# Kernel tuning notes

Measured on AMD Instinct MI355X. Metric: run time of the kernel, lower is better.

Reference implementation:

```python
import jax, jax.numpy as jnp
import numpy as np


def _ste_binarize(w):
    # tanh + (binary - tanh).detach()  ->  forward: (tanh(w) > 0) == (w > 0) as 0/1 float
    t = jnp.tanh(w)
    b = (t > 0).astype(w.dtype)
    return t + jax.lax.stop_gradient(b - t)


def setup_inputs() -> dict:
    key = jax.random.key(0)
    k1, k2, k3 = jax.random.split(key, 3)
    B, S, D_IN, D_OUT = 8, 2048, 4096, 4096
    x = jax.random.normal(k1, (B, S, D_IN), dtype=jnp.float32)
    # nn.Linear default init: U(-1/sqrt(in), 1/sqrt(in))
    bound = 1.0 / np.sqrt(D_IN)
    w_pos = jax.random.uniform(k2, (D_OUT, D_IN), minval=-bound, maxval=bound, dtype=jnp.float32)
    w_neg = jax.random.uniform(k3, (D_OUT, D_IN), minval=-bound, maxval=bound, dtype=jnp.float32)
    return {"x": x, "w_pos": w_pos, "w_neg": w_neg}


def reference(x, w_pos, w_neg):
    wp = _ste_binarize(w_pos)  # [O, I] 0/1 values
    wn = _ste_binarize(w_neg)
    # y = x @ wp.T - x @ wn.T ; fuse the subtract into one GEMM-equivalent expr
    y_pos = jnp.einsum('bsi,oi->bso', x, wp)
    y_neg = jnp.einsum('bsi,oi->bso', x, wn)
    return y_pos - y_neg
```

## Files before the change

kernel.cpp:

```cpp
#include <hip/hip_runtime.h>
#include <stdint.h>


#define M_DIM 16384
#define N_DIM 4096
#define K_DIM 4096

#define BM 256
#define BN 256
#define BK 32
#define NT (K_DIM / BK)
#define SLOT_U16 16384
#define LDS_BYTES 131072

typedef unsigned short u16;
typedef __attribute__((ext_vector_type(8))) __bf16 bf16x8;
typedef __attribute__((ext_vector_type(4))) float f32x4;

__device__ __forceinline__ u16 f2bf(float f) {
    unsigned u = __float_as_uint(f);
    u += 0x7FFFu + ((u >> 16) & 1u);
    return (u16)(u >> 16);
}

__global__ void cvt_x_kernel(const float4* __restrict__ x, uint2* __restrict__ xb, int n4) {
    int i = blockIdx.x * 256 + threadIdx.x;
    if (i >= n4) return;
    float4 v = x[i];
    uint2 r;
    r.x = (unsigned)f2bf(v.x) | ((unsigned)f2bf(v.y) << 16);
    r.y = (unsigned)f2bf(v.z) | ((unsigned)f2bf(v.w) << 16);
    xb[i] = r;
}

__device__ __forceinline__ unsigned enc_w(float a, float b) {
    int s = (int)(a > 0.f) - (int)(b > 0.f);
    return s == 0 ? 0u : (s > 0 ? 0x3F80u : 0xBF80u);
}

__global__ void binarize_w_kernel(const float4* __restrict__ wp, const float4* __restrict__ wn,
                                  uint2* __restrict__ wb, int n4) {
    int i = blockIdx.x * 256 + threadIdx.x;
    if (i >= n4) return;
    float4 p = wp[i];
    float4 q = wn[i];
    uint2 r;
    r.x = enc_w(p.x, q.x) | (enc_w(p.y, q.y) << 16);
    r.y = enc_w(p.z, q.z) | (enc_w(p.w, q.w) << 16);
    wb[i] = r;
}

__device__ __forceinline__ void gload16(const u16* g, u16* l) {
    __builtin_amdgcn_global_load_lds(
        (const __attribute__((address_space(1))) void*)g,
        (__attribute__((address_space(3))) void*)l,
        16, 0, 0);
}

__launch_bounds__(512, 2)
__global__ void gemm_bin_kernel(const u16* __restrict__ A,
                                const u16* __restrict__ B,
                                float* __restrict__ C) {
    extern __shared__ __align__(16) u16 lds[];

    const int t    = threadIdx.x;
    const int lane = t & 63;
    const int wid  = t >> 6;
    const int wrow = wid >> 2;
    const int wcol = wid & 3;
    const int l15  = lane & 15;
    const int quad = lane >> 4;

    const int orig = blockIdx.y * 16 + blockIdx.x;
    const int wgid = (orig & 7) * 128 + (orig >> 3);
    const int bm = (wgid >> 4) * BM;
    const int bn = (wgid & 15) * BN;

    const int srow = ((t >> 6) << 4) | (t & 15);
    const int skk  = ((t >> 4) & 3) * 8;
    const u16* gA0 = A + (size_t)(bm + srow) * K_DIM + skk;
    const u16* gA1 = gA0 + (size_t)128 * K_DIM;
    const u16* gB0 = B + (size_t)(bn + srow) * K_DIM + skk;
    const u16* gB1 = gB0 + (size_t)128 * K_DIM;
    const int ldst = t * 8;

#define STAGE_A(S, K0) do { u16* d_ = lds + (S) * SLOT_U16 + ldst;            \
        gload16(gA0 + (K0), d_); gload16(gA1 + (K0), d_ + 4096); } while (0)
#define STAGE_B(S, K0) do { u16* d_ = lds + (S) * SLOT_U16 + 8192 + ldst;     \
        gload16(gB0 + (K0), d_); gload16(gB1 + (K0), d_ + 4096); } while (0)

    const int aoff = (wrow * 8) * 512 + quad * 128 + l15 * 8;
    const int boff = (wcol * 4) * 512 + quad * 128 + l15 * 8;

    f32x4 acc[8][4];
#pragma unroll
    for (int i = 0; i < 8; ++i)
#pragma unroll
        for (int j = 0; j < 4; ++j) acc[i][j] = (f32x4){0.f, 0.f, 0.f, 0.f};

    STAGE_A(0, 0);      STAGE_B(0, 0);
    STAGE_A(1, BK);     STAGE_B(1, BK);
    STAGE_A(2, 2 * BK); STAGE_B(2, 2 * BK);
    asm volatile("s_waitcnt vmcnt(8)" ::: "memory");
    __builtin_amdgcn_s_barrier();

    for (int tt = 0; tt < NT; ++tt) {
        const u16* As = lds + (tt & 3) * SLOT_U16;
        const u16* Bs = As + 8192;
        const bool doStage = (tt + 3) < NT;
        const int ss = (tt + 3) & 3;
        const int sk = (tt + 3) * BK;

        bf16x8 af[8], bf[4];
#pragma unroll
        for (int i = 0; i < 4; ++i) af[i] = *(const bf16x8*)(As + aoff + i * 512);
#pragma unroll
        for (int i = 0; i < 4; ++i) bf[i] = *(const bf16x8*)(Bs + boff + i * 512);
        if (doStage) STAGE_A(ss, sk);
#pragma unroll
        for (int i = 4; i < 8; ++i) af[i] = *(const bf16x8*)(As + aoff + i * 512);
        if (doStage) STAGE_B(ss, sk);

        __builtin_amdgcn_s_setprio(1);
#pragma unroll
        for (int mi = 0; mi < 8; ++mi)
#pragma unroll
            for (int ni = 0; ni < 4; ++ni)
                acc[mi][ni] = __builtin_amdgcn_mfma_f32_16x16x32_bf16(
                    af[mi], bf[ni], acc[mi][ni], 0, 0, 0);
        __builtin_amdgcn_s_setprio(0);

        if (tt < NT - 3)       asm volatile("s_waitcnt vmcnt(8)" ::: "memory");
        else if (tt == NT - 3) asm volatile("s_waitcnt vmcnt(4)" ::: "memory");
        else if (tt == NT - 2) asm volatile("s_waitcnt vmcnt(0)" ::: "memory");
        __builtin_amdgcn_s_barrier();
    }

#pragma unroll
    for (int mi = 0; mi < 8; ++mi) {
        const int row0 = bm + wrow * 128 + mi * 16 + quad * 4;
#pragma unroll
        for (int ni = 0; ni < 4; ++ni) {
            const int col = bn + wcol * 64 + ni * 16 + l15;
#pragma unroll
            for (int r = 0; r < 4; ++r)
                C[(size_t)(row0 + r) * N_DIM + col] = acc[mi][ni][r];
        }
    }
#undef STAGE_A
#undef STAGE_B
}

extern "C" void kernel_launch(void* const* d_in, const int* in_sizes, int n_in,
                              void* d_out, int out_size, void* d_ws, size_t ws_size,
                              hipStream_t stream) {
    const float* x  = (const float*)d_in[0];
    const float* wp = (const float*)d_in[1];
    const float* wn = (const float*)d_in[2];
    float* out = (float*)d_out;

    u16* xb = (u16*)d_ws;
    u16* wb = (u16*)((char*)d_ws + (size_t)M_DIM * K_DIM * sizeof(u16));

    const int nx4 = M_DIM * K_DIM / 4;
    cvt_x_kernel<<<nx4 / 256, 256, 0, stream>>>((const float4*)x, (uint2*)xb, nx4);

    const int nw4 = N_DIM * K_DIM / 4;
    binarize_w_kernel<<<nw4 / 256, 256, 0, stream>>>(
        (const float4*)wp, (const float4*)wn, (uint2*)wb, nw4);

    static int s_attr_done = 0;
    if (!s_attr_done) {
        hipFuncSetAttribute((const void*)gemm_bin_kernel,
                            hipFuncAttributeMaxDynamicSharedMemorySize, LDS_BYTES);
        s_attr_done = 1;
    }
    dim3 grid(N_DIM / BN, M_DIM / BM);
    gemm_bin_kernel<<<grid, 512, LDS_BYTES, stream>>>(xb, wb, out);
}
```

Measured before the change: 1.021 ms.

## Restructure GEMM main loop into 8-wave ping-pong schedule with half-tile stages

Replaces the 4-slot, BK=32 pipelined loop with a double-buffered BK=64 scheme. Each buffer is split into half-K A/B tiles. Each step interleaves LDS fragment reads, async global-to-LDS stages and 16-MFMA clusters, separated by explicit barriers, sched_barriers and priority toggles, in the style of a ping-pong warp schedule. The aim is to overlap memory traffic with MFMA work more tightly. The cost is many more workgroup barriers per K step and a shallower prefetch depth.

```diff
diff --git a/kernel.cpp b/kernel.cpp
--- a/kernel.cpp
+++ b/kernel.cpp
@@ -8,9 +8,8 @@
 
 #define BM 256
 #define BN 256
-#define BK 32
-#define NT (K_DIM / BK)
-#define SLOT_U16 16384
+#define NT 64
+#define HBUF_U16 8192
 #define LDS_BYTES 131072
 
 typedef unsigned short u16;
@@ -84,13 +83,19 @@
     const u16* gB1 = gB0 + (size_t)128 * K_DIM;
     const int ldst = t * 8;
 
-#define STAGE_A(S, K0) do { u16* d_ = lds + (S) * SLOT_U16 + ldst;            \
-        gload16(gA0 + (K0), d_); gload16(gA1 + (K0), d_ + 4096); } while (0)
-#define STAGE_B(S, K0) do { u16* d_ = lds + (S) * SLOT_U16 + 8192 + ldst;     \
-        gload16(gB0 + (K0), d_); gload16(gB1 + (K0), d_ + 4096); } while (0)
-
-    const int aoff = (wrow * 8) * 512 + quad * 128 + l15 * 8;
-    const int boff = (wcol * 4) * 512 + quad * 128 + l15 * 8;
+#define STAGE_A(S, KC, U) do {                                                 \
+        u16* d_ = lds + ((S) * 4 + (KC) * 2 + 0) * HBUF_U16 + ldst;            \
+        const u16* s_ = gA0 + (U) * 64 + (KC) * 32;                            \
+        gload16(s_, d_); gload16(s_ + (size_t)128 * K_DIM, d_ + 4096);         \
+    } while (0)
+#define STAGE_B(S, KC, U) do {                                                 \
+        u16* d_ = lds + ((S) * 4 + (KC) * 2 + 1) * HBUF_U16 + ldst;            \
+        const u16* s_ = gB0 + (U) * 64 + (KC) * 32;                            \
+        gload16(s_, d_); gload16(s_ + (size_t)128 * K_DIM, d_ + 4096);         \
+    } while (0)
+
+    const int aoffs = wrow * 4096 + quad * 128 + l15 * 8;
+    const int boffs = wcol * 2048 + quad * 128 + l15 * 8;
 
     f32x4 acc[8][4];
 #pragma unroll
@@ -98,42 +103,82 @@
 #pragma unroll
         for (int j = 0; j < 4; ++j) acc[i][j] = (f32x4){0.f, 0.f, 0.f, 0.f};
 
-    STAGE_A(0, 0);      STAGE_B(0, 0);
-    STAGE_A(1, BK);     STAGE_B(1, BK);
-    STAGE_A(2, 2 * BK); STAGE_B(2, 2 * BK);
-    asm volatile("s_waitcnt vmcnt(8)" ::: "memory");
+    STAGE_A(0, 0, 0); STAGE_B(0, 0, 0);
+    STAGE_A(0, 1, 0); STAGE_B(0, 1, 0);
+    asm volatile("s_waitcnt vmcnt(4)" ::: "memory");
     __builtin_amdgcn_s_barrier();
 
-    for (int tt = 0; tt < NT; ++tt) {
-        const u16* As = lds + (tt & 3) * SLOT_U16;
-        const u16* Bs = As + 8192;
-        const bool doStage = (tt + 3) < NT;
-        const int ss = (tt + 3) & 3;
-        const int sk = (tt + 3) * BK;
-
-        bf16x8 af[8], bf[4];
-#pragma unroll
-        for (int i = 0; i < 4; ++i) af[i] = *(const bf16x8*)(As + aoff + i * 512);
-#pragma unroll
-        for (int i = 0; i < 4; ++i) bf[i] = *(const bf16x8*)(Bs + boff + i * 512);
-        if (doStage) STAGE_A(ss, sk);
-#pragma unroll
-        for (int i = 4; i < 8; ++i) af[i] = *(const bf16x8*)(As + aoff + i * 512);
-        if (doStage) STAGE_B(ss, sk);
-
-        __builtin_amdgcn_s_setprio(1);
-#pragma unroll
-        for (int mi = 0; mi < 8; ++mi)
-#pragma unroll
-            for (int ni = 0; ni < 4; ++ni)
-                acc[mi][ni] = __builtin_amdgcn_mfma_f32_16x16x32_bf16(
-                    af[mi], bf[ni], acc[mi][ni], 0, 0, 0);
-        __builtin_amdgcn_s_setprio(0);
-
-        if (tt < NT - 3)       asm volatile("s_waitcnt vmcnt(8)" ::: "memory");
-        else if (tt == NT - 3) asm volatile("s_waitcnt vmcnt(4)" ::: "memory");
-        else if (tt == NT - 2) asm volatile("s_waitcnt vmcnt(0)" ::: "memory");
-        __builtin_amdgcn_s_barrier();
+#define MFMA16(MB, AF, BF)                                                     \
+    _Pragma("unroll")                                                          \
+    for (int mi = 0; mi < 4; ++mi)                                             \
+        _Pragma("unroll")                                                      \
+        for (int ni = 0; ni < 4; ++ni)                                         \
+            acc[(MB) + mi][ni] = __builtin_amdgcn_mfma_f32_16x16x32_bf16(      \
+                (AF)[mi], (BF)[ni], acc[(MB) + mi][ni], 0, 0, 0)
+
+#define STEP(S, T) do {                                                        \
+        const u16* As0 = lds + ((S) * 4 + 0) * HBUF_U16;                       \
+        const u16* Bs0 = lds + ((S) * 4 + 1) * HBUF_U16;                       \
+        const u16* As1 = lds + ((S) * 4 + 2) * HBUF_U16;                       \
+        const u16* Bs1 = lds + ((S) * 4 + 3) * HBUF_U16;                       \
+        const bool st_ = (T) + 1 < NT;                                         \
+        bf16x8 afL[4], afH[4], bfr[4];                                         \
+                                               \
+        _Pragma("unroll")                                                      \
+        for (int i = 0; i < 4; ++i) {                                          \
+            afL[i] = *(const bf16x8*)(As0 + aoffs + i * 512);                  \
+            bfr[i] = *(const bf16x8*)(Bs0 + boffs + i * 512);                  \
+        }                                                                      \
+        if (st_) STAGE_A(1 - (S), 0, (T) + 1);                                 \
+        __builtin_amdgcn_sched_barrier(0);                                     \
+        __builtin_amdgcn_s_barrier();                                          \
+        __builtin_amdgcn_s_setprio(1);                                         \
+        MFMA16(0, afL, bfr);                                                   \
+        __builtin_amdgcn_s_setprio(0);                                         \
+        __builtin_amdgcn_s_barrier();                                          \
+                                               \
+        _Pragma("unroll")                                                      \
+        for (int i = 0; i < 4; ++i)                                            \
+            afH[i] = *(const bf16x8*)(As0 + aoffs + (4 + i) * 512);            \
+        if (st_) STAGE_B(1 - (S), 0, (T) + 1);                                 \
+        __builtin_amdgcn_sched_barrier(0);                                     \
+        __builtin_amdgcn_s_barrier();                                          \
+        __builtin_amdgcn_s_setprio(1);                                         \
+        MFMA16(4, afH, bfr);                                                   \
+        __builtin_amdgcn_s_setprio(0);                                         \
+        if (st_) asm volatile("s_waitcnt vmcnt(4)" ::: "memory");              \
+        else     asm volatile("s_waitcnt vmcnt(0)" ::: "memory");              \
+        __builtin_amdgcn_s_barrier();                                          \
+                                               \
+        _Pragma("unroll")                                                      \
+        for (int i = 0; i < 4; ++i) {                                          \
+            afL[i] = *(const bf16x8*)(As1 + aoffs + i * 512);                  \
+            bfr[i] = *(const bf16x8*)(Bs1 + boffs + i * 512);                  \
+        }                                                                      \
+        if (st_) STAGE_A(1 - (S), 1, (T) + 1);                                 \
+        __builtin_amdgcn_sched_barrier(0);                                     \
+        __builtin_amdgcn_s_barrier();                                          \
+        __builtin_amdgcn_s_setprio(1);                                         \
+        MFMA16(0, afL, bfr);                                                   \
+        __builtin_amdgcn_s_setprio(0);                                         \
+        __builtin_amdgcn_s_barrier();                                          \
+                                               \
+        _Pragma("unroll")                                                      \
+        for (int i = 0; i < 4; ++i)                                            \
+            afH[i] = *(const bf16x8*)(As1 + aoffs + (4 + i) * 512);            \
+        if (st_) STAGE_B(1 - (S), 1, (T) + 1);                                 \
+        __builtin_amdgcn_sched_barrier(0);                                     \
+        __builtin_amdgcn_s_barrier();                                          \
+        __builtin_amdgcn_s_setprio(1);                                         \
+        MFMA16(4, afH, bfr);                                                   \
+        __builtin_amdgcn_s_setprio(0);                                         \
+        if (st_) asm volatile("s_waitcnt vmcnt(4)" ::: "memory");              \
+        __builtin_amdgcn_s_barrier();                                          \
+    } while (0)
+
+    for (int tt = 0; tt < NT; tt += 2) {
+        STEP(0, tt);
+        STEP(1, tt + 1);
     }
 
 #pragma unroll
@@ -147,6 +192,8 @@
                 C[(size_t)(row0 + r) * N_DIM + col] = acc[mi][ni][r];
         }
     }
+#undef STEP
+#undef MFMA16
 #undef STAGE_A
 #undef STAGE_B
 }
```

Result: no change. 1.029 ms (+0.7%).
